# Optimization experiments

Hardware: AMD Instinct MI355X
Metric: run time of the kernel (lower is better)

Reference implementation:

```python
import jax, jax.numpy as jnp
import numpy as np

B, T, N, IN_DIM, H, C, L, S, P = 64, 13, 325, 2, 64, 4, 2, 4, 12
NC = S * N  # combined temporal-graph node count per batch element


def _make_adj(rng, n, density=0.03):
    mask = rng.random((n, n)) < density
    return (mask * rng.random((n, n))).astype(np.float32)


def _combine(adj, s, forward):
    n = adj.shape[0]
    out = np.zeros((n * s, n * s), np.float32)
    for i in range(s):
        out[i * n:(i + 1) * n, i * n:(i + 1) * n] = adj
        if forward and i < s - 1:
            out[i * n:(i + 1) * n, (i + 1) * n:(i + 2) * n] = np.eye(n, dtype=np.float32)
    return out


def _checkpoints(s, t):
    mark, cp = s, []
    while mark < t:
        cp.append(mark)
        mark += s - 1
    if cp[-1] != t:
        cp.append(t)
    return cp


def setup_inputs():
    key = jax.random.key(0)
    ks = jax.random.split(key, 20)
    rng = np.random.default_rng(0)
    adj = _make_adj(rng, N)
    pea = _make_adj(rng, N)
    sc = 0.05
    inp = {
        'inputs': jax.random.normal(ks[0], (B, T, N, IN_DIM), jnp.float32),
        'adj_fwd': jnp.asarray(_combine(adj, S, True)),
        'adj_bwd': jnp.asarray(_combine(adj, S, False)),
        'pea_fwd': jnp.asarray(_combine(pea, S, True)),
        'pea_bwd': jnp.asarray(_combine(pea, S, False)),
        'w_in': sc * jax.random.normal(ks[1], (IN_DIM, H), jnp.float32),
        'b_in': jnp.zeros((H,), jnp.float32),
        'res_w': sc * jax.random.normal(ks[2], (S,), jnp.float32),
        'res_b': jnp.zeros((), jnp.float32),
        'gconv_w': sc * jax.random.normal(ks[3], (S,), jnp.float32),
        'gconv_b': jnp.zeros((), jnp.float32),
        'gate1_w': sc * jax.random.normal(ks[4], (H, H), jnp.float32),
        'gate1_b': jnp.zeros((H,), jnp.float32),
        'gate2_w': sc * jax.random.normal(ks[5], (H, H * C), jnp.float32),
        'gate2_b': jnp.zeros((H * C,), jnp.float32),
        'reduce_w': sc * jax.random.normal(ks[6], (C * H, H), jnp.float32),
        'reduce_b': jnp.zeros((H,), jnp.float32),
        'gcn_adj_w': sc * jax.random.normal(ks[7], (C, L, 2, H, H), jnp.float32),
        'gcn_adj_b': jnp.zeros((C, L, H), jnp.float32),
        'gcn_pea_w': sc * jax.random.normal(ks[8], (C, L, 2, H, H), jnp.float32),
        'gcn_pea_b': jnp.zeros((C, L, H), jnp.float32),
        'out_conv_w': sc * jax.random.normal(ks[9], (P,), jnp.float32),
        'out_conv_b': jnp.zeros((P,), jnp.float32),
        'out_lin_w': sc * jax.random.normal(ks[10], (H, 1), jnp.float32),
        'out_lin_b': jnp.zeros((1,), jnp.float32),
    }
    return inp


def _gcn_stack(feats, W, b, A_f, A_b, n_out):
    # feats [B, S*N, H]; W [L, 2, H, H]; weighted message passing over both supports
    h = feats
    for l in range(W.shape[0]):
        mf = jnp.einsum('nm,bmh->bnh', A_f, h)
        mb = jnp.einsum('nm,bmh->bnh', A_b, h)
        h = jax.nn.relu(mf @ W[l, 0] + mb @ W[l, 1] + b[l])
    return h[:, -n_out:, :]  # last snapshot's nodes -> [B, N, H]


def reference(inputs, adj_fwd, adj_bwd, pea_fwd, pea_bwd, w_in, b_in, res_w, res_b,
              gconv_w, gconv_b, gate1_w, gate1_b, gate2_w, gate2_b, reduce_w, reduce_b,
              gcn_adj_w, gcn_adj_b, gcn_pea_w, gcn_pea_b, out_conv_w, out_conv_b,
              out_lin_w, out_lin_b):
    b_, t_, n_, _ = inputs.shape
    h_ = w_in.shape[1]
    s_ = res_w.shape[0]
    c_ = gcn_adj_w.shape[0]
    x = inputs @ w_in + b_in  # [B, T, N, H]
    last = None
    left = 0
    for idx, right in enumerate(_checkpoints(s_, t_)):
        fs = x[:, left:right] if idx == 0 else jnp.concatenate([last, x[:, left:right]], axis=1)  # [B,S,N,H]
        gf = (jnp.einsum('s,bsnh->bnh', gconv_w, fs) + gconv_b).reshape(b_ * n_, h_)
        residual = jnp.einsum('s,bsnh->bnh', res_w, fs) + res_b  # [B,N,H]
        feats = fs.reshape(b_, s_ * n_, h_)
        ca = jnp.concatenate(
            [_gcn_stack(feats, gcn_adj_w[c], gcn_adj_b[c], adj_fwd, adj_bwd, n_) for c in range(c_)],
            axis=-1).reshape(b_ * n_, c_ * h_)
        cp = jnp.concatenate(
            [_gcn_stack(feats, gcn_pea_w[c], gcn_pea_b[c], pea_fwd, pea_bwd, n_) for c in range(c_)],
            axis=-1).reshape(b_ * n_, c_ * h_)
        gate = jax.nn.sigmoid(jax.nn.relu(gf @ gate1_w + gate1_b) @ gate2_w + gate2_b)
        gr = gate * ca + (1.0 - gate) * cp
        gr = (gr @ reduce_w + reduce_b).reshape(b_, n_, h_)
        cr = gr + residual
        # nn.LayerNorm([B, N, H], elementwise_affine=False): normalize over whole tensor
        mu = jnp.mean(cr)
        var = jnp.var(cr)
        last = ((cr - mu) * jax.lax.rsqrt(var + 1e-5))[:, None]  # [B,1,N,H]
        left = right
    # 1x1 conv 1->pred_len over channel dim, then linear H->1
    out = jax.nn.relu(out_conv_w.reshape(1, -1, 1, 1) * last + out_conv_b.reshape(1, -1, 1, 1))
    out = out @ out_lin_w + out_lin_b  # [B, pred_len, N, 1]
    return out
```

## Files before the change

kernel.cpp:

```cpp
#include <hip/hip_runtime.h>
#include <hip/hip_bf16.h>
#include <math.h>

#define B_    64
#define T_    13
#define N_    325
#define H_    64
#define C_    4
#define L_    2
#define S_    4
#define P_    12
#define KCP   4
#define M_    (B_*N_)
#define ADJLD 1300
#define NNZCAP 64
#define WPITCH 72
#define MTP   264
#define RTP   264
#define NBLK  1300

typedef short bfrag __attribute__((ext_vector_type(8)));
typedef float f32x4 __attribute__((ext_vector_type(4)));

__device__ __forceinline__ void fma4(float4& a, float s, float4 x) {
    a.x += s * x.x; a.y += s * x.y; a.z += s * x.z; a.w += s * x.w;
}
__device__ __forceinline__ ushort bf_rne(float f) {
    unsigned u = __float_as_uint(f);
    return (ushort)((u + 0x7fffu + ((u >> 16) & 1u)) >> 16);
}
__device__ __forceinline__ uint2 pack_bf4(float4 v) {
    unsigned a = __float_as_uint(v.x), b = __float_as_uint(v.y);
    unsigned c = __float_as_uint(v.z), d = __float_as_uint(v.w);
    a = (a + 0x7fffu + ((a >> 16) & 1u)) >> 16;
    b = (b + 0x7fffu + ((b >> 16) & 1u)) >> 16;
    c = (c + 0x7fffu + ((c >> 16) & 1u)) >> 16;
    d = (d + 0x7fffu + ((d >> 16) & 1u)) >> 16;
    return make_uint2(a | (b << 16), c | (d << 16));
}
__device__ __forceinline__ float4 unpack_bf4(uint2 p) {
    return make_float4(__uint_as_float(p.x << 16),
                       __uint_as_float(p.x & 0xffff0000u),
                       __uint_as_float(p.y << 16),
                       __uint_as_float(p.y & 0xffff0000u));
}
__device__ __forceinline__ int rl_i(int v, int l) {
    return __builtin_amdgcn_readlane(v, l);
}
__device__ __forceinline__ float rl_f(float v, int l) {
    return __uint_as_float(__builtin_amdgcn_readlane(__float_as_uint(v), l));
}
__device__ __forceinline__ float bfu(ushort u) {
    return __uint_as_float((unsigned)u << 16);
}

__global__ void k_build_sparse(const float* __restrict__ A,
                               int* __restrict__ cnt, int* __restrict__ cols,
                               float* __restrict__ vals) {
    int n    = blockIdx.x;
    int lane = threadIdx.x;
    const float* row = A + (size_t)n * ADJLD;
    int c = 0;
    for (int c0 = 0; c0 < 384; c0 += 64) {
        int col = c0 + lane;
        float v = (col < N_) ? row[col] : 0.f;
        unsigned long long m = __ballot(v != 0.f);
        int idx = c + __popcll(m & ((1ull << lane) - 1ull));
        if (v != 0.f && idx < NNZCAP) {
            cols[n * NNZCAP + idx] = col;
            vals[n * NNZCAP + idx] = v;
        }
        c += __popcll(m);
    }
    if (c + lane < NNZCAP) {
        cols[n * NNZCAP + c + lane] = 0;
        vals[n * NNZCAP + c + lane] = 0.f;
    }
    if (lane == 0) cnt[n] = (c < NNZCAP) ? c : NNZCAP;
}

__global__ void k_ginit(const float* __restrict__ inp,
                        const float* __restrict__ w_in, const float* __restrict__ b_in,
                        ushort* __restrict__ g_init4) {
    int idx = blockIdx.x * 256 + threadIdx.x;
    if (idx >= 4 * M_ * H_) return;
    int h  = idx & 63;
    int r  = idx >> 6;
    int it = r / M_;
    int m  = r - it * M_;
    int b  = m / N_, n = m % N_;
    int tt = 3 * it + 3;
    const float* ip = inp + ((size_t)(b * T_ + tt) * N_ + n) * 2;
    g_init4[idx] = bf_rne(ip[0] * w_in[h] + ip[1] * w_in[H_ + h] + b_in[h]);
}

__global__ void k_prep_w(const float* __restrict__ gadj_w,
                         const float* __restrict__ gpea_w,
                         ushort* __restrict__ WT) {
    int mat = blockIdx.x;
    int layer = mat >> 3, sm = mat & 7;
    int stack = sm >> 2, c = sm & 3;
    const float* w0 = (stack ? gpea_w : gadj_w) + (size_t)((c * L_ + layer) * 2) * 4096;
    const float* w1 = w0 + 4096;
    for (int i = 0; i < 16; ++i) {
        int e = threadIdx.x + i * 256;
        int k = e >> 6, n = e & 63;
        WT[((size_t)mat * 64 + n) * WPITCH + k] = bf_rne(w0[e] + w1[e]);
    }
}

__global__ void k_prep_rt(const float* __restrict__ reduce_w,
                          ushort* __restrict__ RT) {
    for (int i = 0; i < 64; ++i) {
        int e = threadIdx.x + i * 256;
        int k = e >> 6, n = e & 63;
        RT[(size_t)n * RTP + k] = bf_rne(reduce_w[e]);
    }
}

__global__ void k_prep_gate(const float* __restrict__ W1, const float* __restrict__ W2,
                            ushort* __restrict__ W1T, ushort* __restrict__ W2T) {
    int t = threadIdx.x;
    if (blockIdx.x == 0) {
        for (int i = 0; i < 16; ++i) {
            int e = t + i * 256;
            int k = e >> 6, n = e & 63;
            W1T[(size_t)n * WPITCH + k] = bf_rne(W1[e]);
        }
    } else {
        for (int i = 0; i < 64; ++i) {
            int e = t + i * 256;
            int k = e >> 8, n = e & 255;
            W2T[(size_t)n * WPITCH + k] = bf_rne(W2[e]);
        }
    }
}

__global__ __launch_bounds__(256, 4) void k_layer1(
    const int*   __restrict__ cnt,
    const int*   __restrict__ cols,
    const float* __restrict__ vals,
    const ushort* __restrict__ g_init4,
    int it0,
    const ushort* __restrict__ WT,
    const float* __restrict__ badj, const float* __restrict__ bpea,
    ushort* __restrict__ G1a4, ushort* __restrict__ G1p4)
{
    __shared__ __align__(16) ushort MaH[32 * WPITCH];
    __shared__ __align__(16) ushort MpH[32 * WPITCH];
    int t = threadIdx.x, lane = t & 63, w = t >> 6;
    int itk = blockIdx.x / 656;
    int lx  = blockIdx.x - itk * 656;
    int vb = (lx & 7) * 82 + (lx >> 3);
    if (vb >= 650) return;
    int m0 = vb * 32;
    const ushort* g_init = g_init4 + (size_t)(it0 + itk) * M_ * H_;
    ushort* G1a = G1a4 + (size_t)itk * M_ * 256;
    ushort* G1p = G1p4 + (size_t)itk * M_ * 256;
    int q = lane >> 4, ml = lane & 15;
    int colg = w * 16 + ml;

    int mcA[8]; float mvA[8]; int mcP[8]; float mvP[8]; int jmv[8]; int nrow[8];
    #pragma unroll
    for (int rl = 0; rl < 8; ++rl) {
        int m = m0 + w * 8 + rl;
        int n = m % N_;
        nrow[rl] = n;
        mcA[rl] = cols[n * NNZCAP + lane];
        mvA[rl] = vals[n * NNZCAP + lane];
        mcP[rl] = cols[(N_ + n) * NNZCAP + lane];
        mvP[rl] = vals[(N_ + n) * NNZCAP + lane];
        jmv[rl] = max(cnt[n], cnt[N_ + n]);
    }

    #pragma unroll
    for (int g = 0; g < 4; ++g) {
        int rA = w * 8 + g, rB = rA + 4;
        int mA = m0 + rA,   mB = m0 + rB;
        int nA = nrow[g],   nB = nrow[g + 4];
        const ushort* gA = g_init + (size_t)(mA - nA) * H_ + lane;
        const ushort* gB = g_init + (size_t)(mB - nB) * H_ + lane;
        int jm = __builtin_amdgcn_readfirstlane(max(jmv[g], jmv[g + 4]));
        float aA0 = 0.f, aB0 = 0.f, aA1 = 0.f, aB1 = 0.f;
        for (int j = 0; j < jm; j += 2) {
            int c0 = rl_i(mcA[g], j),     c1 = rl_i(mcA[g], j + 1);
            int c2 = rl_i(mcA[g + 4], j), c3 = rl_i(mcA[g + 4], j + 1);
            int c4 = rl_i(mcP[g], j),     c5 = rl_i(mcP[g], j + 1);
            int c6 = rl_i(mcP[g + 4], j), c7 = rl_i(mcP[g + 4], j + 1);
            float v0 = rl_f(mvA[g], j),     v1 = rl_f(mvA[g], j + 1);
            float v2 = rl_f(mvA[g + 4], j), v3 = rl_f(mvA[g + 4], j + 1);
            float v4 = rl_f(mvP[g], j),     v5 = rl_f(mvP[g], j + 1);
            float v6 = rl_f(mvP[g + 4], j), v7 = rl_f(mvP[g + 4], j + 1);
            aA0 += v0 * bfu(gA[c0 * H_]) + v1 * bfu(gA[c1 * H_]);
            aB0 += v2 * bfu(gB[c2 * H_]) + v3 * bfu(gB[c3 * H_]);
            aA1 += v4 * bfu(gA[c4 * H_]) + v5 * bfu(gA[c5 * H_]);
            aB1 += v6 * bfu(gB[c6 * H_]) + v7 * bfu(gB[c7 * H_]);
        }
        MaH[rA * WPITCH + lane] = bf_rne(aA0);
        MaH[rB * WPITCH + lane] = bf_rne(aB0);
        MpH[rA * WPITCH + lane] = bf_rne(aA1);
        MpH[rB * WPITCH + lane] = bf_rne(aB1);
    }
    __syncthreads();

    bfrag B0c = *(const bfrag*)&WT[(size_t)colg * WPITCH + q * 8];
    bfrag B1c = *(const bfrag*)&WT[(size_t)colg * WPITCH + 32 + q * 8];
    #pragma unroll
    for (int sc = 0; sc < 8; ++sc) {
        int stack = sc >> 2, c = sc & 3;
        bfrag B0n = B0c, B1n = B1c;
        if (sc < 7) {
            B0n = *(const bfrag*)&WT[((size_t)(sc + 1) * 64 + colg) * WPITCH + q * 8];
            B1n = *(const bfrag*)&WT[((size_t)(sc + 1) * 64 + colg) * WPITCH + 32 + q * 8];
        }
        const ushort* Msrc = stack ? MpH : MaH;
        float bv = (stack ? bpea : badj)[c * L_ * H_ + colg];
        ushort* Gout = stack ? G1p : G1a;
        #pragma unroll
        for (int r = 0; r < 2; ++r) {
            bfrag A0 = *(const bfrag*)&Msrc[(16 * r + ml) * WPITCH + q * 8];
            bfrag A1 = *(const bfrag*)&Msrc[(16 * r + ml) * WPITCH + 32 + q * 8];
            f32x4 acc = {0.f, 0.f, 0.f, 0.f};
            acc = __builtin_amdgcn_mfma_f32_16x16x32_bf16(A0, B0c, acc, 0, 0, 0);
            acc = __builtin_amdgcn_mfma_f32_16x16x32_bf16(A1, B1c, acc, 0, 0, 0);
            #pragma unroll
            for (int j = 0; j < 4; ++j) {
                float v = acc[j] + bv;
                v = v > 0.f ? v : 0.f;
                Gout[(size_t)(m0 + 16 * r + q * 4 + j) * 256 + c * 64 + colg] = bf_rne(v);
            }
        }
        B0c = B0n; B1c = B1n;
    }
}

__global__ __launch_bounds__(256, 5) void k_mix(
    const float* __restrict__ inp,
    const float* __restrict__ w_in, const float* __restrict__ b_in,
    const float* __restrict__ gconv_w, const float* __restrict__ gconv_b,
    const float* __restrict__ res_w,   const float* __restrict__ res_b,
    const float* __restrict__ cr_in, int it,
    const ushort* __restrict__ W1T, const float* __restrict__ b1,
    const ushort* __restrict__ W2T, const float* __restrict__ b2,
    const int*   __restrict__ cnt,
    const int*   __restrict__ cols,
    const float* __restrict__ vals,
    const ushort* __restrict__ G1a, const ushort* __restrict__ G1p,
    const ushort* __restrict__ WT,
    const float* __restrict__ badj, const float* __restrict__ bpea,
    const ushort* __restrict__ RT,
    const float* __restrict__ reduce_b,
    float* __restrict__ cr,
    const float* __restrict__ partials_in,
    float* __restrict__ partials)
{
    __shared__ __align__(16) ushort MtA[16 * MTP];
    __shared__ __align__(16) ushort MtP[16 * MTP];
    __shared__ __align__(16) ushort Gf[16 * WPITCH];
    __shared__ __align__(16) ushort Gr[16 * WPITCH];
    __shared__ float RES[16 * 68];
    __shared__ float red[8];
    int t = threadIdx.x, lane = t & 63, w = t >> 6;
    int vb = (blockIdx.x & 7) * 163 + (blockIdx.x >> 3);
    if (vb >= NBLK) return;
    int m0 = vb * 16;
    int q = lane >> 4, ml = lane & 15;
    int colg = w * 16 + ml;

    int mcA[4]; float mvA[4]; int mcP[4]; float mvP[4]; int jmv[4]; int nrw[4];
    #pragma unroll
    for (int rl = 0; rl < 4; ++rl) {
        int m = m0 + w * 4 + rl;
        int n = m % N_;
        nrw[rl] = n;
        mcA[rl] = cols[n * NNZCAP + lane];
        mvA[rl] = vals[n * NNZCAP + lane];
        mcP[rl] = cols[(N_ + n) * NNZCAP + lane];
        mvP[rl] = vals[(N_ + n) * NNZCAP + lane];
        jmv[rl] = max(cnt[n], cnt[N_ + n]);
    }

    float mu = 0.f, rs = 0.f;
    if (it > 0) {
        float* REDS = (float*)MtA;
        float a = 0.f, b = 0.f;
        for (int i = t; i < NBLK; i += 256) { a += partials_in[i]; b += partials_in[NBLK + i]; }
        REDS[t] = a; REDS[256 + t] = b;
        __syncthreads();
        for (int off = 128; off > 0; off >>= 1) {
            if (t < off) { REDS[t] += REDS[t + off]; REDS[256 + t] += REDS[256 + t + off]; }
            __syncthreads();
        }
        const float inv = 1.f / (float)(M_ * H_);
        mu = REDS[0] * inv;
        float var = REDS[256] * inv - mu * mu;
        rs = rsqrtf(var + 1e-5f);
        __syncthreads();
    }

    {
        float wa = w_in[lane], wb = w_in[H_ + lane], bi = b_in[lane];
        float gw0 = gconv_w[0], gw1 = gconv_w[1], gw2 = gconv_w[2], gw3 = gconv_w[3];
        float rw0 = res_w[0],   rw1 = res_w[1],   rw2 = res_w[2],   rw3 = res_w[3];
        float gb = gconv_b[0],  rb = res_b[0];
        int t1 = (it == 0) ? 1 : (3 * it + 1);
        for (int i = 0; i < 4; ++i) {
            int r = i * 4 + w;
            int m = m0 + r;
            int b = m / N_, n = m % N_;
            const float* ipb = inp + ((size_t)b * T_ * N_ + n) * 2;
            float v0;
            if (it > 0) v0 = (cr_in[(size_t)m * H_ + lane] - mu) * rs;
            else        v0 = ipb[0] * wa + ipb[1] * wb + bi;
            const float* ip1 = ipb + (size_t)t1 * N_ * 2;
            const float* ip2 = ip1 + (size_t)N_ * 2;
            const float* ip3 = ip2 + (size_t)N_ * 2;
            float v1 = ip1[0] * wa + ip1[1] * wb + bi;
            float v2 = ip2[0] * wa + ip2[1] * wb + bi;
            float v3 = ip3[0] * wa + ip3[1] * wb + bi;
            Gf[r * WPITCH + lane] = bf_rne(gb + gw0 * v0 + gw1 * v1 + gw2 * v2 + gw3 * v3);
            RES[r * 68 + lane]    = rb + rw0 * v0 + rw1 * v1 + rw2 * v2 + rw3 * v3;
        }
    }
    __syncthreads();

    {
        bfrag A0 = *(const bfrag*)&Gf[ml * WPITCH + q * 8];
        bfrag A1 = *(const bfrag*)&Gf[ml * WPITCH + 32 + q * 8];
        bfrag B0 = *(const bfrag*)&W1T[(size_t)colg * WPITCH + q * 8];
        bfrag B1 = *(const bfrag*)&W1T[(size_t)colg * WPITCH + 32 + q * 8];
        f32x4 acc = {0.f, 0.f, 0.f, 0.f};
        acc = __builtin_amdgcn_mfma_f32_16x16x32_bf16(A0, B0, acc, 0, 0, 0);
        acc = __builtin_amdgcn_mfma_f32_16x16x32_bf16(A1, B1, acc, 0, 0, 0);
        float bb = b1[colg];
        #pragma unroll
        for (int j = 0; j < 4; ++j) {
            float v = acc[j] + bb;
            v = v > 0.f ? v : 0.f;
            Gr[(q * 4 + j) * WPITCH + colg] = bf_rne(v);
        }
    }
    __syncthreads();

    f32x4 gsv[4];
    {
        bfrag A0 = *(const bfrag*)&Gr[ml * WPITCH + q * 8];
        bfrag A1 = *(const bfrag*)&Gr[ml * WPITCH + 32 + q * 8];
        #pragma unroll
        for (int c = 0; c < 4; ++c) {
            bfrag B0 = *(const bfrag*)&W2T[(size_t)(c * 64 + colg) * WPITCH + q * 8];
            bfrag B1 = *(const bfrag*)&W2T[(size_t)(c * 64 + colg) * WPITCH + 32 + q * 8];
            f32x4 acc = {0.f, 0.f, 0.f, 0.f};
            acc = __builtin_amdgcn_mfma_f32_16x16x32_bf16(A0, B0, acc, 0, 0, 0);
            acc = __builtin_amdgcn_mfma_f32_16x16x32_bf16(A1, B1, acc, 0, 0, 0);
            float bb = b2[c * 64 + colg];
            #pragma unroll
            for (int j = 0; j < 4; ++j)
                gsv[c][j] = 1.f / (1.f + expf(-(acc[j] + bb)));
        }
    }

    #pragma unroll
    for (int g = 0; g < 2; ++g) {
        int r0 = w * 4 + 2 * g;
        int ma = m0 + r0, mb = ma + 1;
        int na = nrw[2 * g], nb = nrw[2 * g + 1];
        const ushort* ga = G1a + (size_t)(ma - na) * 256 + lane * 4;
        const ushort* gb = G1a + (size_t)(mb - nb) * 256 + lane * 4;
        const ushort* pa = G1p + (size_t)(ma - na) * 256 + lane * 4;
        const ushort* pb = G1p + (size_t)(mb - nb) * 256 + lane * 4;
        int jm = __builtin_amdgcn_readfirstlane(max(jmv[2 * g], jmv[2 * g + 1]));
        float4 a0 = make_float4(0.f,0.f,0.f,0.f), a1 = make_float4(0.f,0.f,0.f,0.f);
        float4 p0 = make_float4(0.f,0.f,0.f,0.f), p1 = make_float4(0.f,0.f,0.f,0.f);
        for (int j = 0; j < jm; j += 2) {
            int ca0 = rl_i(mcA[2 * g], j),     ca1 = rl_i(mcA[2 * g], j + 1);
            int cb0 = rl_i(mcA[2 * g + 1], j), cb1 = rl_i(mcA[2 * g + 1], j + 1);
            int da0 = rl_i(mcP[2 * g], j),     da1 = rl_i(mcP[2 * g], j + 1);
            int db0 = rl_i(mcP[2 * g + 1], j), db1 = rl_i(mcP[2 * g + 1], j + 1);
            float va0 = rl_f(mvA[2 * g], j),     va1 = rl_f(mvA[2 * g], j + 1);
            float vb0 = rl_f(mvA[2 * g + 1], j), vb1 = rl_f(mvA[2 * g + 1], j + 1);
            float wa0 = rl_f(mvP[2 * g], j),     wa1 = rl_f(mvP[2 * g], j + 1);
            float wb0 = rl_f(mvP[2 * g + 1], j), wb1 = rl_f(mvP[2 * g + 1], j + 1);
            fma4(a0, va0, unpack_bf4(*(const uint2*)&ga[ca0 * 256]));
            fma4(a0, va1, unpack_bf4(*(const uint2*)&ga[ca1 * 256]));
            fma4(a1, vb0, unpack_bf4(*(const uint2*)&gb[cb0 * 256]));
            fma4(a1, vb1, unpack_bf4(*(const uint2*)&gb[cb1 * 256]));
            fma4(p0, wa0, unpack_bf4(*(const uint2*)&pa[da0 * 256]));
            fma4(p0, wa1, unpack_bf4(*(const uint2*)&pa[da1 * 256]));
            fma4(p1, wb0, unpack_bf4(*(const uint2*)&pb[db0 * 256]));
            fma4(p1, wb1, unpack_bf4(*(const uint2*)&pb[db1 * 256]));
        }
        *(uint2*)&MtA[r0 * MTP + lane * 4]       = pack_bf4(a0);
        *(uint2*)&MtA[(r0 + 1) * MTP + lane * 4] = pack_bf4(a1);
        *(uint2*)&MtP[r0 * MTP + lane * 4]       = pack_bf4(p0);
        *(uint2*)&MtP[(r0 + 1) * MTP + lane * 4] = pack_bf4(p1);
    }
    __syncthreads();

    const ushort* WT1 = WT + (size_t)8 * 64 * WPITCH;
    f32x4 res[4];
    bfrag B0c = *(const bfrag*)&WT1[(size_t)colg * WPITCH + q * 8];
    bfrag B1c = *(const bfrag*)&WT1[(size_t)colg * WPITCH + 32 + q * 8];
    #pragma unroll
    for (int sc = 0; sc < 8; ++sc) {
        int stack = sc >> 2, c = sc & 3;
        bfrag B0n = B0c, B1n = B1c;
        if (sc < 7) {
            B0n = *(const bfrag*)&WT1[((size_t)(sc + 1) * 64 + colg) * WPITCH + q * 8];
            B1n = *(const bfrag*)&WT1[((size_t)(sc + 1) * 64 + colg) * WPITCH + 32 + q * 8];
        }
        const ushort* Msrc = stack ? MtP : MtA;
        float bv = (stack ? bpea : badj)[(c * L_ + 1) * H_ + colg];
        bfrag A0 = *(const bfrag*)&Msrc[ml * MTP + c * 64 + q * 8];
        bfrag A1 = *(const bfrag*)&Msrc[ml * MTP + c * 64 + 32 + q * 8];
        f32x4 acc = {0.f, 0.f, 0.f, 0.f};
        acc = __builtin_amdgcn_mfma_f32_16x16x32_bf16(A0, B0c, acc, 0, 0, 0);
        acc = __builtin_amdgcn_mfma_f32_16x16x32_bf16(A1, B1c, acc, 0, 0, 0);
        #pragma unroll
        for (int j = 0; j < 4; ++j) {
            float v = acc[j] + bv;
            v = v > 0.f ? v : 0.f;
            if (stack == 0) res[c][j] = gsv[c][j] * v;
            else            res[c][j] += (1.f - gsv[c][j]) * v;
        }
        B0c = B0n; B1c = B1n;
    }

    bfrag RF[8];
    #pragma unroll
    for (int kc = 0; kc < 8; ++kc)
        RF[kc] = *(const bfrag*)&RT[(size_t)colg * RTP + kc * 32 + q * 8];
    f32x4 rv;
    #pragma unroll
    for (int j = 0; j < 4; ++j)
        rv[j] = RES[(q * 4 + j) * 68 + colg];

    __syncthreads();
    #pragma unroll
    for (int c = 0; c < 4; ++c)
        #pragma unroll
        for (int j = 0; j < 4; ++j)
            MtA[(q * 4 + j) * MTP + c * 64 + colg] = bf_rne(res[c][j]);
    __syncthreads();

    f32x4 racc = {0.f, 0.f, 0.f, 0.f};
    #pragma unroll
    for (int kc = 0; kc < 8; ++kc) {
        bfrag A0 = *(const bfrag*)&MtA[ml * MTP + kc * 32 + q * 8];
        racc = __builtin_amdgcn_mfma_f32_16x16x32_bf16(A0, RF[kc], racc, 0, 0, 0);
    }

    float bi = reduce_b[colg];
    float s = 0.f, s2 = 0.f;
    #pragma unroll
    for (int j = 0; j < 4; ++j) {
        int m = m0 + q * 4 + j;
        float v = racc[j] + bi + rv[j];
        cr[(size_t)m * 64 + colg] = v;
        s += v; s2 += v * v;
    }
    #pragma unroll
    for (int off = 32; off > 0; off >>= 1) {
        s  += __shfl_xor(s, off);
        s2 += __shfl_xor(s2, off);
    }
    if (lane == 0) { red[w] = s; red[4 + w] = s2; }
    __syncthreads();
    if (t == 0) partials[vb]        = red[0] + red[1] + red[2] + red[3];
    if (t == 1) partials[NBLK + vb] = red[4] + red[5] + red[6] + red[7];
}

__global__ __launch_bounds__(64) void k_out(
    const float* __restrict__ cr, const float* __restrict__ partials,
    const float* __restrict__ ocw, const float* __restrict__ ocb,
    const float* __restrict__ olw, const float* __restrict__ olb,
    float* __restrict__ out) {
    int t = threadIdx.x;
    float a = 0.f, b2s = 0.f;
    for (int i = t; i < NBLK; i += 64) { a += partials[i]; b2s += partials[NBLK + i]; }
    #pragma unroll
    for (int off = 32; off > 0; off >>= 1) {
        a   += __shfl_xor(a, off);
        b2s += __shfl_xor(b2s, off);
    }
    const float inv = 1.f / (float)(M_ * H_);
    float mu  = a * inv;
    float var = b2s * inv - mu * mu;
    float rs  = rsqrtf(var + 1e-5f);

    int m = blockIdx.x * 64 + t;
    int b = m / N_, n = m % N_;
    float cw[P_], cb[P_], acc[P_];
    #pragma unroll
    for (int p = 0; p < P_; ++p) { cw[p] = ocw[p]; cb[p] = ocb[p]; acc[p] = 0.f; }
    const float* lr = cr + (size_t)m * H_;
    for (int h4 = 0; h4 < 64; h4 += 4) {
        float4 lv4 = *(const float4*)&lr[h4];
        float4 wv4 = *(const float4*)&olw[h4];
        float lv[4] = {(lv4.x - mu) * rs, (lv4.y - mu) * rs,
                       (lv4.z - mu) * rs, (lv4.w - mu) * rs};
        float wv[4] = {wv4.x, wv4.y, wv4.z, wv4.w};
        #pragma unroll
        for (int e = 0; e < 4; ++e) {
            float lvv = lv[e], wvv = wv[e];
            #pragma unroll
            for (int p = 0; p < P_; ++p) {
                float u = cw[p] * lvv + cb[p];
                u = u > 0.f ? u : 0.f;
                acc[p] += u * wvv;
            }
        }
    }
    float ob = olb[0];
    #pragma unroll
    for (int p = 0; p < P_; ++p)
        out[(size_t)(b * P_ + p) * N_ + n] = acc[p] + ob;
}

extern "C" void kernel_launch(void* const* d_in, const int* in_sizes, int n_in,
                              void* d_out, int out_size, void* d_ws, size_t ws_size,
                              hipStream_t stream) {
    const float* inp      = (const float*)d_in[0];
    const float* adj_fwd  = (const float*)d_in[1];
    const float* pea_fwd  = (const float*)d_in[3];
    const float* w_in     = (const float*)d_in[5];
    const float* b_in     = (const float*)d_in[6];
    const float* res_w    = (const float*)d_in[7];
    const float* res_b    = (const float*)d_in[8];
    const float* gconv_w  = (const float*)d_in[9];
    const float* gconv_b  = (const float*)d_in[10];
    const float* gate1_w  = (const float*)d_in[11];
    const float* gate1_b  = (const float*)d_in[12];
    const float* gate2_w  = (const float*)d_in[13];
    const float* gate2_b  = (const float*)d_in[14];
    const float* reduce_w = (const float*)d_in[15];
    const float* reduce_b = (const float*)d_in[16];
    const float* gadj_w   = (const float*)d_in[17];
    const float* gadj_b   = (const float*)d_in[18];
    const float* gpea_w   = (const float*)d_in[19];
    const float* gpea_b   = (const float*)d_in[20];
    const float* ocw      = (const float*)d_in[21];
    const float* ocb      = (const float*)d_in[22];
    const float* olw      = (const float*)d_in[23];
    const float* olb      = (const float*)d_in[24];
    float* out = (float*)d_out;

    float* ws       = (float*)d_ws;
    float* cr       = ws;
    float* partials = cr + (size_t)M_ * H_;
    int*   scnt  = (int*)(partials + 2 * NBLK);
    int*   scols = scnt + 2 * N_;
    float* svals = (float*)(scols + 2 * N_ * NNZCAP);
    ushort* G1a4 = (ushort*)(svals + 2 * N_ * NNZCAP);
    ushort* G1p4 = G1a4 + 2 * (size_t)M_ * 256;
    ushort* g_init4 = G1p4 + 2 * (size_t)M_ * 256;
    ushort* WT   = g_init4 + 4 * (size_t)M_ * H_;
    WT = (ushort*)(((uintptr_t)WT + 15) & ~(uintptr_t)15);
    ushort* RT   = WT + 16 * 64 * WPITCH;
    ushort* W1T  = RT + 64 * RTP;
    ushort* W2T  = W1T + 64 * WPITCH;

    k_build_sparse<<<N_, 64, 0, stream>>>(adj_fwd, scnt,      scols,              svals);
    k_build_sparse<<<N_, 64, 0, stream>>>(pea_fwd, scnt + N_, scols + N_*NNZCAP,  svals + N_*NNZCAP);
    k_ginit<<<(4 * M_ * H_) / 256, 256, 0, stream>>>(inp, w_in, b_in, g_init4);
    k_prep_w<<<16, 256, 0, stream>>>(gadj_w, gpea_w, WT);
    k_prep_rt<<<1, 256, 0, stream>>>(reduce_w, RT);
    k_prep_gate<<<2, 256, 0, stream>>>(gate1_w, gate2_w, W1T, W2T);

    for (int half = 0; half < 2; ++half) {
        k_layer1<<<2 * 656, 256, 0, stream>>>(
            scnt, scols, svals, g_init4, half * 2,
            WT, gadj_b, gpea_b, G1a4, G1p4);
        for (int it = half * 2; it < half * 2 + 2; ++it) {
            int slot = it & 1;
            k_mix<<<1304, 256, 0, stream>>>(
                inp, w_in, b_in, gconv_w, gconv_b, res_w, res_b, cr, it,
                W1T, gate1_b, W2T, gate2_b,
                scnt, scols, svals,
                G1a4 + (size_t)slot * M_ * 256, G1p4 + (size_t)slot * M_ * 256,
                WT, gadj_b, gpea_b, RT, reduce_b, cr, partials, partials);
        }
    }

    k_out<<<N_, 64, 0, stream>>>(cr, partials, ocw, ocb, olw, olb, out);
}
```

Before: 495.5 us.

## Fuse setup kernels, widen sparse gather ILP, use shuffle reduction in mix

Merges six small setup and prep kernels into one launch, with block ranges assigned to sparse build, input projection and weight transposes. The sparse gather loops in k_layer1 and k_mix now process four rows per pass instead of two, giving more independent loads in flight. The LayerNorm partial-sum reduction in k_mix switches from a shared-memory tree with many barriers to wavefront shuffles. k_mix launch bounds drop from 5 to 4 waves, trading occupancy for more registers for the wider gather. The wider gather also iterates up to the maximum nnz over four rows, which may add wasted iterations.

Result: no change. 503.7 us (+1.7%).

```diff
diff --git a/kernel.cpp b/kernel.cpp
--- a/kernel.cpp
+++ b/kernel.cpp
@@ -54,84 +54,78 @@
     return __uint_as_float((unsigned)u << 16);
 }
 
-__global__ void k_build_sparse(const float* __restrict__ A,
-                               int* __restrict__ cnt, int* __restrict__ cols,
-                               float* __restrict__ vals) {
-    int n    = blockIdx.x;
-    int lane = threadIdx.x;
-    const float* row = A + (size_t)n * ADJLD;
-    int c = 0;
-    for (int c0 = 0; c0 < 384; c0 += 64) {
-        int col = c0 + lane;
-        float v = (col < N_) ? row[col] : 0.f;
-        unsigned long long m = __ballot(v != 0.f);
-        int idx = c + __popcll(m & ((1ull << lane) - 1ull));
-        if (v != 0.f && idx < NNZCAP) {
-            cols[n * NNZCAP + idx] = col;
-            vals[n * NNZCAP + idx] = v;
-        }
-        c += __popcll(m);
-    }
-    if (c + lane < NNZCAP) {
-        cols[n * NNZCAP + c + lane] = 0;
-        vals[n * NNZCAP + c + lane] = 0.f;
-    }
-    if (lane == 0) cnt[n] = (c < NNZCAP) ? c : NNZCAP;
-}
-
-__global__ void k_ginit(const float* __restrict__ inp,
-                        const float* __restrict__ w_in, const float* __restrict__ b_in,
-                        ushort* __restrict__ g_init4) {
-    int idx = blockIdx.x * 256 + threadIdx.x;
-    if (idx >= 4 * M_ * H_) return;
-    int h  = idx & 63;
-    int r  = idx >> 6;
-    int it = r / M_;
-    int m  = r - it * M_;
-    int b  = m / N_, n = m % N_;
-    int tt = 3 * it + 3;
-    const float* ip = inp + ((size_t)(b * T_ + tt) * N_ + n) * 2;
-    g_init4[idx] = bf_rne(ip[0] * w_in[h] + ip[1] * w_in[H_ + h] + b_in[h]);
-}
-
-__global__ void k_prep_w(const float* __restrict__ gadj_w,
-                         const float* __restrict__ gpea_w,
-                         ushort* __restrict__ WT) {
-    int mat = blockIdx.x;
-    int layer = mat >> 3, sm = mat & 7;
-    int stack = sm >> 2, c = sm & 3;
-    const float* w0 = (stack ? gpea_w : gadj_w) + (size_t)((c * L_ + layer) * 2) * 4096;
-    const float* w1 = w0 + 4096;
-    for (int i = 0; i < 16; ++i) {
-        int e = threadIdx.x + i * 256;
-        int k = e >> 6, n = e & 63;
-        WT[((size_t)mat * 64 + n) * WPITCH + k] = bf_rne(w0[e] + w1[e]);
-    }
-}
-
-__global__ void k_prep_rt(const float* __restrict__ reduce_w,
-                          ushort* __restrict__ RT) {
-    for (int i = 0; i < 64; ++i) {
-        int e = threadIdx.x + i * 256;
-        int k = e >> 6, n = e & 63;
-        RT[(size_t)n * RTP + k] = bf_rne(reduce_w[e]);
-    }
-}
-
-__global__ void k_prep_gate(const float* __restrict__ W1, const float* __restrict__ W2,
-                            ushort* __restrict__ W1T, ushort* __restrict__ W2T) {
-    int t = threadIdx.x;
-    if (blockIdx.x == 0) {
+__global__ void k_setup(
+    const float* __restrict__ adj_fwd, const float* __restrict__ pea_fwd,
+    const float* __restrict__ inp,
+    const float* __restrict__ w_in, const float* __restrict__ b_in,
+    const float* __restrict__ gadj_w, const float* __restrict__ gpea_w,
+    const float* __restrict__ reduce_w,
+    const float* __restrict__ gate1_w, const float* __restrict__ gate2_w,
+    int* __restrict__ cnt, int* __restrict__ cols, float* __restrict__ vals,
+    ushort* __restrict__ g_init4, ushort* __restrict__ WT,
+    ushort* __restrict__ RT, ushort* __restrict__ W1T, ushort* __restrict__ W2T)
+{
+    int bid = blockIdx.x, t = threadIdx.x;
+    if (bid >= 182) {
+        int idx = (bid - 182) * 256 + t;
+        if (idx >= 4 * M_ * H_) return;
+        int h  = idx & 63;
+        int r  = idx >> 6;
+        int it = r / M_;
+        int m  = r - it * M_;
+        int b  = m / N_, n = m % N_;
+        int tt = 3 * it + 3;
+        const float* ip = inp + ((size_t)(b * T_ + tt) * N_ + n) * 2;
+        g_init4[idx] = bf_rne(ip[0] * w_in[h] + ip[1] * w_in[H_ + h] + b_in[h]);
+    } else if (bid < 163) {
+        int lane = t & 63, w = t >> 6;
+        int row = bid * 4 + w;
+        if (row >= 2 * N_) return;
+        int mat = (row >= N_) ? 1 : 0;
+        int n   = row - mat * N_;
+        const float* A = mat ? pea_fwd : adj_fwd;
+        const float* rp = A + (size_t)n * ADJLD;
+        int* cw   = cols + (size_t)row * NNZCAP;
+        float* vw = vals + (size_t)row * NNZCAP;
+        int c = 0;
+        for (int c0 = 0; c0 < 384; c0 += 64) {
+            int col = c0 + lane;
+            float v = (col < N_) ? rp[col] : 0.f;
+            unsigned long long mmask = __ballot(v != 0.f);
+            int idx = c + __popcll(mmask & ((1ull << lane) - 1ull));
+            if (v != 0.f && idx < NNZCAP) { cw[idx] = col; vw[idx] = v; }
+            c += __popcll(mmask);
+        }
+        if (c + lane < NNZCAP) { cw[c + lane] = 0; vw[c + lane] = 0.f; }
+        if (lane == 0) cnt[row] = (c < NNZCAP) ? c : NNZCAP;
+    } else if (bid == 163) {
+        for (int i = 0; i < 64; ++i) {
+            int e = t + i * 256;
+            int k = e >> 6, n = e & 63;
+            RT[(size_t)n * RTP + k] = bf_rne(reduce_w[e]);
+        }
+    } else if (bid < 180) {
+        int mat = bid - 164;
+        int layer = mat >> 3, sm = mat & 7;
+        int stack = sm >> 2, c = sm & 3;
+        const float* w0 = (stack ? gpea_w : gadj_w) + (size_t)((c * L_ + layer) * 2) * 4096;
+        const float* w1 = w0 + 4096;
         for (int i = 0; i < 16; ++i) {
             int e = t + i * 256;
             int k = e >> 6, n = e & 63;
-            W1T[(size_t)n * WPITCH + k] = bf_rne(W1[e]);
+            WT[((size_t)mat * 64 + n) * WPITCH + k] = bf_rne(w0[e] + w1[e]);
+        }
+    } else if (bid == 180) {
+        for (int i = 0; i < 16; ++i) {
+            int e = t + i * 256;
+            int k = e >> 6, n = e & 63;
+            W1T[(size_t)n * WPITCH + k] = bf_rne(gate1_w[e]);
         }
     } else {
         for (int i = 0; i < 64; ++i) {
             int e = t + i * 256;
             int k = e >> 8, n = e & 255;
-            W2T[(size_t)n * WPITCH + k] = bf_rne(W2[e]);
+            W2T[(size_t)n * WPITCH + k] = bf_rne(gate2_w[e]);
         }
     }
 }
@@ -174,32 +168,35 @@
     }
 
     #pragma unroll
-    for (int g = 0; g < 4; ++g) {
-        int rA = w * 8 + g, rB = rA + 4;
-        int mA = m0 + rA,   mB = m0 + rB;
-        int nA = nrow[g],   nB = nrow[g + 4];
-        const ushort* gA = g_init + (size_t)(mA - nA) * H_ + lane;
-        const ushort* gB = g_init + (size_t)(mB - nB) * H_ + lane;
-        int jm = __builtin_amdgcn_readfirstlane(max(jmv[g], jmv[g + 4]));
-        float aA0 = 0.f, aB0 = 0.f, aA1 = 0.f, aB1 = 0.f;
+    for (int gg = 0; gg < 2; ++gg) {
+        const ushort* gp[4];
+        #pragma unroll
+        for (int k = 0; k < 4; ++k) {
+            int ii = 2 * gg + (k >> 1) * 4 + (k & 1);
+            int m  = m0 + w * 8 + ii;
+            gp[k] = g_init + (size_t)(m - nrow[ii]) * H_ + lane;
+        }
+        int jm = __builtin_amdgcn_readfirstlane(
+            max(max(jmv[2*gg], jmv[2*gg+1]), max(jmv[2*gg+4], jmv[2*gg+5])));
+        float aA[4] = {0.f,0.f,0.f,0.f}, aP[4] = {0.f,0.f,0.f,0.f};
         for (int j = 0; j < jm; j += 2) {
-            int c0 = rl_i(mcA[g], j),     c1 = rl_i(mcA[g], j + 1);
-            int c2 = rl_i(mcA[g + 4], j), c3 = rl_i(mcA[g + 4], j + 1);
-            int c4 = rl_i(mcP[g], j),     c5 = rl_i(mcP[g], j + 1);
-            int c6 = rl_i(mcP[g + 4], j), c7 = rl_i(mcP[g + 4], j + 1);
-            float v0 = rl_f(mvA[g], j),     v1 = rl_f(mvA[g], j + 1);
-            float v2 = rl_f(mvA[g + 4], j), v3 = rl_f(mvA[g + 4], j + 1);
-            float v4 = rl_f(mvP[g], j),     v5 = rl_f(mvP[g], j + 1);
-            float v6 = rl_f(mvP[g + 4], j), v7 = rl_f(mvP[g + 4], j + 1);
-            aA0 += v0 * bfu(gA[c0 * H_]) + v1 * bfu(gA[c1 * H_]);
-            aB0 += v2 * bfu(gB[c2 * H_]) + v3 * bfu(gB[c3 * H_]);
-            aA1 += v4 * bfu(gA[c4 * H_]) + v5 * bfu(gA[c5 * H_]);
-            aB1 += v6 * bfu(gB[c6 * H_]) + v7 * bfu(gB[c7 * H_]);
-        }
-        MaH[rA * WPITCH + lane] = bf_rne(aA0);
-        MaH[rB * WPITCH + lane] = bf_rne(aB0);
-        MpH[rA * WPITCH + lane] = bf_rne(aA1);
-        MpH[rB * WPITCH + lane] = bf_rne(aB1);
+            #pragma unroll
+            for (int k = 0; k < 4; ++k) {
+                int ii = 2 * gg + (k >> 1) * 4 + (k & 1);
+                int c0 = rl_i(mcA[ii], j), c1 = rl_i(mcA[ii], j + 1);
+                int d0 = rl_i(mcP[ii], j), d1 = rl_i(mcP[ii], j + 1);
+                float v0 = rl_f(mvA[ii], j), v1 = rl_f(mvA[ii], j + 1);
+                float u0 = rl_f(mvP[ii], j), u1 = rl_f(mvP[ii], j + 1);
+                aA[k] += v0 * bfu(gp[k][c0 * H_]) + v1 * bfu(gp[k][c1 * H_]);
+                aP[k] += u0 * bfu(gp[k][d0 * H_]) + u1 * bfu(gp[k][d1 * H_]);
+            }
+        }
+        #pragma unroll
+        for (int k = 0; k < 4; ++k) {
+            int rr = w * 8 + 2 * gg + (k >> 1) * 4 + (k & 1);
+            MaH[rr * WPITCH + lane] = bf_rne(aA[k]);
+            MpH[rr * WPITCH + lane] = bf_rne(aP[k]);
+        }
     }
     __syncthreads();
 
@@ -234,7 +231,7 @@
     }
 }
 
-__global__ __launch_bounds__(256, 5) void k_mix(
+__global__ __launch_bounds__(256, 4) void k_mix(
     const float* __restrict__ inp,
     const float* __restrict__ w_in, const float* __restrict__ b_in,
     const float* __restrict__ gconv_w, const float* __restrict__ gconv_b,
@@ -282,20 +279,21 @@
 
     float mu = 0.f, rs = 0.f;
     if (it > 0) {
-        float* REDS = (float*)MtA;
         float a = 0.f, b = 0.f;
         for (int i = t; i < NBLK; i += 256) { a += partials_in[i]; b += partials_in[NBLK + i]; }
-        REDS[t] = a; REDS[256 + t] = b;
+        #pragma unroll
+        for (int off = 32; off > 0; off >>= 1) {
+            a += __shfl_xor(a, off);
+            b += __shfl_xor(b, off);
+        }
+        if (lane == 0) { red[w] = a; red[4 + w] = b; }
         __syncthreads();
-        for (int off = 128; off > 0; off >>= 1) {
-            if (t < off) { REDS[t] += REDS[t + off]; REDS[256 + t] += REDS[256 + t + off]; }
-            __syncthreads();
-        }
+        a = red[0] + red[1] + red[2] + red[3];
+        b = red[4] + red[5] + red[6] + red[7];
         const float inv = 1.f / (float)(M_ * H_);
-        mu = REDS[0] * inv;
-        float var = REDS[256] * inv - mu * mu;
+        mu = a * inv;
+        float var = b * inv - mu * mu;
         rs = rsqrtf(var + 1e-5f);
-        __syncthreads();
     }
 
     {
@@ -360,40 +358,42 @@
         }
     }
 
-    #pragma unroll
-    for (int g = 0; g < 2; ++g) {
-        int r0 = w * 4 + 2 * g;
-        int ma = m0 + r0, mb = ma + 1;
-        int na = nrw[2 * g], nb = nrw[2 * g + 1];
-        const ushort* ga = G1a + (size_t)(ma - na) * 256 + lane * 4;
-        const ushort* gb = G1a + (size_t)(mb - nb) * 256 + lane * 4;
-        const ushort* pa = G1p + (size_t)(ma - na) * 256 + lane * 4;
-        const ushort* pb = G1p + (size_t)(mb - nb) * 256 + lane * 4;
-        int jm = __builtin_amdgcn_readfirstlane(max(jmv[2 * g], jmv[2 * g + 1]));
-        float4 a0 = make_float4(0.f,0.f,0.f,0.f), a1 = make_float4(0.f,0.f,0.f,0.f);
-        float4 p0 = make_float4(0.f,0.f,0.f,0.f), p1 = make_float4(0.f,0.f,0.f,0.f);
+    {
+        const ushort *ga[4], *pa[4];
+        #pragma unroll
+        for (int rr = 0; rr < 4; ++rr) {
+            int m = m0 + w * 4 + rr;
+            size_t base = (size_t)(m - nrw[rr]) * 256 + lane * 4;
+            ga[rr] = G1a + base;
+            pa[rr] = G1p + base;
+        }
+        int jm = __builtin_amdgcn_readfirstlane(
+            max(max(jmv[0], jmv[1]), max(jmv[2], jmv[3])));
+        float4 av[4], pv[4];
+        #pragma unroll
+        for (int rr = 0; rr < 4; ++rr) {
+            av[rr] = make_float4(0.f,0.f,0.f,0.f);
+            pv[rr] = make_float4(0.f,0.f,0.f,0.f);
+        }
         for (int j = 0; j < jm; j += 2) {
-            int ca0 = rl_i(mcA[2 * g], j),     ca1 = rl_i(mcA[2 * g], j + 1);
-            int cb0 = rl_i(mcA[2 * g + 1], j), cb1 = rl_i(mcA[2 * g + 1], j + 1);
-            int da0 = rl_i(mcP[2 * g], j),     da1 = rl_i(mcP[2 * g], j + 1);
-            int db0 = rl_i(mcP[2 * g + 1], j), db1 = rl_i(mcP[2 * g + 1], j + 1);
-            float va0 = rl_f(mvA[2 * g], j),     va1 = rl_f(mvA[2 * g], j + 1);
-            float vb0 = rl_f(mvA[2 * g + 1], j), vb1 = rl_f(mvA[2 * g + 1], j + 1);
-            float wa0 = rl_f(mvP[2 * g], j),     wa1 = rl_f(mvP[2 * g], j + 1);
-            float wb0 = rl_f(mvP[2 * g + 1], j), wb1 = rl_f(mvP[2 * g + 1], j + 1);
-            fma4(a0, va0, unpack_bf4(*(const uint2*)&ga[ca0 * 256]));
-            fma4(a0, va1, unpack_bf4(*(const uint2*)&ga[ca1 * 256]));
-            fma4(a1, vb0, unpack_bf4(*(const uint2*)&gb[cb0 * 256]));
-            fma4(a1, vb1, unpack_bf4(*(const uint2*)&gb[cb1 * 256]));
-            fma4(p0, wa0, unpack_bf4(*(const uint2*)&pa[da0 * 256]));
-            fma4(p0, wa1, unpack_bf4(*(const uint2*)&pa[da1 * 256]));
-            fma4(p1, wb0, unpack_bf4(*(const uint2*)&pb[db0 * 256]));
-            fma4(p1, wb1, unpack_bf4(*(const uint2*)&pb[db1 * 256]));
-        }
-        *(uint2*)&MtA[r0 * MTP + lane * 4]       = pack_bf4(a0);
-        *(uint2*)&MtA[(r0 + 1) * MTP + lane * 4] = pack_bf4(a1);
-        *(uint2*)&MtP[r0 * MTP + lane * 4]       = pack_bf4(p0);
-        *(uint2*)&MtP[(r0 + 1) * MTP + lane * 4] = pack_bf4(p1);
+            #pragma unroll
+            for (int rr = 0; rr < 4; ++rr) {
+                int c0 = rl_i(mcA[rr], j), c1 = rl_i(mcA[rr], j + 1);
+                int d0 = rl_i(mcP[rr], j), d1 = rl_i(mcP[rr], j + 1);
+                float v0 = rl_f(mvA[rr], j), v1 = rl_f(mvA[rr], j + 1);
+                float u0 = rl_f(mvP[rr], j), u1 = rl_f(mvP[rr], j + 1);
+                fma4(av[rr], v0, unpack_bf4(*(const uint2*)&ga[rr][c0 * 256]));
+                fma4(av[rr], v1, unpack_bf4(*(const uint2*)&ga[rr][c1 * 256]));
+                fma4(pv[rr], u0, unpack_bf4(*(const uint2*)&pa[rr][d0 * 256]));
+                fma4(pv[rr], u1, unpack_bf4(*(const uint2*)&pa[rr][d1 * 256]));
+            }
+        }
+        #pragma unroll
+        for (int rr = 0; rr < 4; ++rr) {
+            int r0 = w * 4 + rr;
+            *(uint2*)&MtA[r0 * MTP + lane * 4] = pack_bf4(av[rr]);
+            *(uint2*)&MtP[r0 * MTP + lane * 4] = pack_bf4(pv[rr]);
+        }
     }
     __syncthreads();
 
@@ -560,12 +560,9 @@
     ushort* W1T  = RT + 64 * RTP;
     ushort* W2T  = W1T + 64 * WPITCH;
 
-    k_build_sparse<<<N_, 64, 0, stream>>>(adj_fwd, scnt,      scols,              svals);
-    k_build_sparse<<<N_, 64, 0, stream>>>(pea_fwd, scnt + N_, scols + N_*NNZCAP,  svals + N_*NNZCAP);
-    k_ginit<<<(4 * M_ * H_) / 256, 256, 0, stream>>>(inp, w_in, b_in, g_init4);
-    k_prep_w<<<16, 256, 0, stream>>>(gadj_w, gpea_w, WT);
-    k_prep_rt<<<1, 256, 0, stream>>>(reduce_w, RT);
-    k_prep_gate<<<2, 256, 0, stream>>>(gate1_w, gate2_w, W1T, W2T);
+    k_setup<<<182 + (4 * M_ * H_) / 256, 256, 0, stream>>>(
+        adj_fwd, pea_fwd, inp, w_in, b_in, gadj_w, gpea_w, reduce_w,
+        gate1_w, gate2_w, scnt, scols, svals, g_init4, WT, RT, W1T, W2T);
 
     for (int half = 0; half < 2; ++half) {
         k_layer1<<<2 * 656, 256, 0, stream>>>(
```
